# Kernel optimization log

Hardware: AMD Instinct MI355X
Metric: run time of the kernel (lower is better)

## Reference

```python
import jax, jax.numpy as jnp
import numpy as np

D_MODEL = 1024
N_HEADS = 16
HEAD_DIM = D_MODEL // N_HEADS
B, S = 2, 2048


def setup_inputs() -> dict:
    key = jax.random.key(0)
    ks = jax.random.split(key, 6)
    scale = 1.0 / np.sqrt(D_MODEL)
    inputs = jax.random.normal(ks[0], (B, S, D_MODEL), dtype=jnp.float32)
    # causal mask: 1.0 where attention is disallowed (strictly upper triangular)
    mask = jnp.triu(jnp.ones((S, S), dtype=jnp.float32), k=1)[None, None, :, :]
    mask = jnp.broadcast_to(mask, (B, 1, S, S))
    Wq = jax.random.normal(ks[1], (D_MODEL, D_MODEL), dtype=jnp.float32) * scale
    Wk = jax.random.normal(ks[2], (D_MODEL, D_MODEL), dtype=jnp.float32) * scale
    Wv = jax.random.normal(ks[3], (D_MODEL, D_MODEL), dtype=jnp.float32) * scale
    Wo = jax.random.normal(ks[4], (D_MODEL, D_MODEL), dtype=jnp.float32) * scale
    z = jnp.zeros((D_MODEL,), dtype=jnp.float32)
    return {"inputs": inputs, "mask": mask, "Wq": Wq, "bq": z, "Wk": Wk,
            "bk": z, "Wv": Wv, "bv": z, "Wo": Wo, "bo": z}


def _split_heads(x):
    b, s, _ = x.shape
    return x.reshape(b, s, N_HEADS, HEAD_DIM).transpose(0, 2, 1, 3)  # [B,H,S,Dh]


def reference(inputs, mask, Wq, bq, Wk, bk, Wv, bv, Wo, bo):
    q = _split_heads(inputs @ Wq + bq)
    k = _split_heads(inputs @ Wk + bk)
    v = _split_heads(inputs @ Wv + bv)
    # scaled dot-product attention with additive big-negative mask
    logits = jnp.einsum('bhqd,bhkd->bhqk', q, k) / jnp.sqrt(
        jnp.asarray(HEAD_DIM, dtype=q.dtype))
    logits = logits + mask * jnp.asarray(-1e9, dtype=q.dtype)
    attn_prob = jax.nn.softmax(logits, axis=-1)  # [B,H,S,S]
    ctx = jnp.einsum('bhqk,bhkd->bhqd', attn_prob, v)
    ctx = ctx.transpose(0, 2, 1, 3).reshape(inputs.shape[0], -1, D_MODEL)
    outputs = ctx @ Wo + bo
    return outputs, attn_prob
```

## Files before the change

### kernel.cpp

```cpp
#include <hip/hip_runtime.h>
#include <cstdint>

namespace {

typedef __attribute__((ext_vector_type(8))) short bf16x8;
typedef __attribute__((ext_vector_type(4))) short bf16x4;
typedef __attribute__((ext_vector_type(4))) float f32x4;

constexpr int D  = 1024;
constexpr int H  = 16;
constexpr int DH = 64;
constexpr int B  = 2;
constexpr int S  = 2048;
constexpr int M  = B * S;
constexpr float SCALE_Q = 0.125f * 1.4426950408889634f;

__device__ inline unsigned short f2bf(float f) {
    union { float f; uint32_t u; } v{f};
    return (unsigned short)((v.u + 0x7fffu + ((v.u >> 16) & 1u)) >> 16);
}

__device__ inline void gload16(const void* g, void* l) {
    __builtin_amdgcn_global_load_lds(
        (const __attribute__((address_space(1))) void*)g,
        (__attribute__((address_space(3))) void*)l, 16, 0, 0);
}

__global__ __launch_bounds__(256) void pack_x(const float* __restrict__ x,
                                              unsigned short* __restrict__ xb) {
    const int i = (blockIdx.x * 256 + threadIdx.x) * 8;
    float4 a = *reinterpret_cast<const float4*>(&x[i]);
    float4 b = *reinterpret_cast<const float4*>(&x[i + 4]);
    bf16x8 o;
    o[0] = f2bf(a.x); o[1] = f2bf(a.y); o[2] = f2bf(a.z); o[3] = f2bf(a.w);
    o[4] = f2bf(b.x); o[5] = f2bf(b.y); o[6] = f2bf(b.z); o[7] = f2bf(b.w);
    *reinterpret_cast<bf16x8*>(&xb[i]) = o;
}

__global__ __launch_bounds__(256) void transpose_w4(
    const float* __restrict__ W0, const float* __restrict__ W1,
    const float* __restrict__ W2, const float* __restrict__ W3,
    unsigned short* __restrict__ WtAll)
{
    __shared__ unsigned short T[64][72];
    const int z = blockIdx.z;
    const float* W = z == 0 ? W0 : (z == 1 ? W1 : (z == 2 ? W2 : W3));
    unsigned short* Wt = WtAll + (size_t)z * D * D;
    const int n0 = blockIdx.x * 64, k0 = blockIdx.y * 64;
    const int t = threadIdx.x;
    #pragma unroll
    for (int i = 0; i < 16; ++i) {
        int idx = i * 256 + t, r = idx >> 6, c = idx & 63;
        T[r][c] = f2bf(W[(size_t)(k0 + r) * D + n0 + c]);
    }
    __syncthreads();
    #pragma unroll
    for (int i = 0; i < 16; ++i) {
        int idx = i * 256 + t, r = idx >> 6, c = idx & 63;
        Wt[(size_t)(n0 + r) * D + k0 + c] = T[c][r];
    }
}

template <int MODE>
__global__ __launch_bounds__(256) void mfma_gemm(
    const unsigned short* __restrict__ A, const unsigned short* __restrict__ Bt,
    const float* __restrict__ b0, const float* __restrict__ b1,
    const float* __restrict__ b2,
    unsigned short* __restrict__ oQ, unsigned short* __restrict__ oK,
    unsigned short* __restrict__ oVt, float* __restrict__ oF)
{
    __shared__ __align__(16) unsigned short As[128 * 64];
    __shared__ __align__(16) unsigned short Bs[128 * 64];
    const int t = threadIdx.x;
    const int lane = t & 63, w = t >> 6;
    const int wr = w >> 1, wc = w & 1;
    const int lo = lane & 15, hi = lane >> 4;
    const int m0 = blockIdx.y * 128, n0 = blockIdx.x * 128;

    f32x4 acc[4][4] = {};

    for (int k0 = 0; k0 < D; k0 += 64) {
        #pragma unroll
        for (int i = 0; i < 4; ++i) {
            const int row = i * 32 + w * 8 + (lane >> 3);
            const int gcol = ((lane & 7) * 8) ^ ((row & 7) * 8);
            gload16(&A[(size_t)(m0 + row) * D + k0 + gcol], &As[i * 2048 + w * 512]);
            gload16(&Bt[(size_t)(n0 + row) * D + k0 + gcol], &Bs[i * 2048 + w * 512]);
        }
        __syncthreads();
        #pragma unroll
        for (int kk = 0; kk < 2; ++kk) {
            bf16x8 a[4], b[4];
            #pragma unroll
            for (int m = 0; m < 4; ++m) {
                const int row = wr * 64 + m * 16 + lo;
                a[m] = *reinterpret_cast<const bf16x8*>(
                    &As[row * 64 + ((kk * 32 + hi * 8) ^ ((row & 7) * 8))]);
            }
            #pragma unroll
            for (int n = 0; n < 4; ++n) {
                const int row = wc * 64 + n * 16 + lo;
                b[n] = *reinterpret_cast<const bf16x8*>(
                    &Bs[row * 64 + ((kk * 32 + hi * 8) ^ ((row & 7) * 8))]);
            }
            #pragma unroll
            for (int m = 0; m < 4; ++m)
                #pragma unroll
                for (int n = 0; n < 4; ++n)
                    acc[m][n] = __builtin_amdgcn_mfma_f32_16x16x32_bf16(a[m], b[n], acc[m][n], 0, 0, 0);
        }
        __syncthreads();
    }

    if (MODE == 0) {
        const int which = n0 >> 10;
        if (which == 2) {
            #pragma unroll
            for (int m = 0; m < 4; ++m) {
                const int row0 = m0 + wr * 64 + m * 16 + hi * 4;
                const int b_ = row0 >> 11, s_ = row0 & (S - 1);
                #pragma unroll
                for (int n = 0; n < 4; ++n) {
                    const int nn = (n0 + wc * 64 + n * 16 + lo) & 1023;
                    const int h_ = nn >> 6, dh = nn & 63;
                    const float bcol = b2[nn];
                    bf16x4 o;
                    #pragma unroll
                    for (int r = 0; r < 4; ++r) o[r] = (short)f2bf(acc[m][n][r] + bcol);
                    *reinterpret_cast<bf16x4*>(
                        &oVt[((size_t)(b_ * H + h_) * DH + dh) * S + s_]) = o;
                }
            }
        } else {
            const float* bs = which == 0 ? b0 : b1;
            unsigned short* op = which == 0 ? oQ : oK;
            const float scale = which == 0 ? SCALE_Q : 1.0f;
            #pragma unroll
            for (int m = 0; m < 4; ++m)
                #pragma unroll
                for (int n = 0; n < 4; ++n) {
                    const int nn = (n0 + wc * 64 + n * 16 + lo) & 1023;
                    const float bcol = bs[nn];
                    const int h_ = nn >> 6, dh = nn & 63;
                    #pragma unroll
                    for (int r = 0; r < 4; ++r) {
                        const int row = m0 + wr * 64 + m * 16 + hi * 4 + r;
                        const int b_ = row >> 11, s_ = row & (S - 1);
                        op[(((size_t)(b_ * H + h_) * S) + s_) * DH + dh] =
                            f2bf((acc[m][n][r] + bcol) * scale);
                    }
                }
        }
    } else {
        #pragma unroll
        for (int m = 0; m < 4; ++m)
            #pragma unroll
            for (int n = 0; n < 4; ++n) {
                const int col = n0 + wc * 64 + n * 16 + lo;
                const float bcol = b0[col];
                #pragma unroll
                for (int r = 0; r < 4; ++r) {
                    const int row = m0 + wr * 64 + m * 16 + hi * 4 + r;
                    oF[(size_t)row * D + col] = acc[m][n][r] + bcol;
                }
            }
    }
}

__global__ __launch_bounds__(256) void attn_fused(
    const unsigned short* __restrict__ Q, const unsigned short* __restrict__ K,
    const unsigned short* __restrict__ Vt, float* __restrict__ P,
    unsigned short* __restrict__ ctxb)
{
    __shared__ __align__(16) float Pf[2][4][16][68];
    const int bh = blockIdx.x;
    const int y = blockIdx.y;
    const int jy = y & 7, ky = y >> 3;
    const int qt = (ky == 0) ? 31 - jy : (ky == 1) ? jy : (ky == 2) ? 23 - jy : 8 + jy;
    const int t = threadIdx.x, lane = t & 63, w = t >> 6;
    const int lo = lane & 15, hi = lane >> 4;
    const int q0 = qt * 64 + w * 16;
    const unsigned short* Qb = Q + (size_t)bh * S * DH;
    const unsigned short* Kb = K + (size_t)bh * S * DH;
    const unsigned short* Vb = Vt + (size_t)bh * DH * S;
    float* Pb = P + (size_t)bh * S * S;

    bf16x8 aq[2];
    #pragma unroll
    for (int kk = 0; kk < 2; ++kk)
        aq[kk] = *reinterpret_cast<const bf16x8*>(&Qb[(size_t)(q0 + lo) * DH + kk * 32 + hi * 8]);

    float li[4];
    {
        float rsum[4] = {0.f, 0.f, 0.f, 0.f};
        for (int jt = 0; jt < qt; ++jt) {
            f32x4 acc[4] = {};
            #pragma unroll
            for (int kk = 0; kk < 2; ++kk)
                #pragma unroll
                for (int n = 0; n < 4; ++n) {
                    bf16x8 bk = *reinterpret_cast<const bf16x8*>(
                        &Kb[(size_t)(jt * 64 + n * 16 + lo) * DH + kk * 32 + hi * 8]);
                    acc[n] = __builtin_amdgcn_mfma_f32_16x16x32_bf16(aq[kk], bk, acc[n], 0, 0, 0);
                }
            #pragma unroll
            for (int n = 0; n < 4; ++n)
                #pragma unroll
                for (int r = 0; r < 4; ++r) rsum[r] += exp2f(acc[n][r]);
        }
        {
            f32x4 acc[4] = {};
            #pragma unroll
            for (int kk = 0; kk < 2; ++kk)
                #pragma unroll
                for (int n = 0; n < 4; ++n) {
                    bf16x8 bk = *reinterpret_cast<const bf16x8*>(
                        &Kb[(size_t)(qt * 64 + n * 16 + lo) * DH + kk * 32 + hi * 8]);
                    acc[n] = __builtin_amdgcn_mfma_f32_16x16x32_bf16(aq[kk], bk, acc[n], 0, 0, 0);
                }
            #pragma unroll
            for (int n = 0; n < 4; ++n) {
                const int j = qt * 64 + n * 16 + lo;
                #pragma unroll
                for (int r = 0; r < 4; ++r) {
                    const float e = exp2f(acc[n][r]);
                    rsum[r] += (j > q0 + hi * 4 + r) ? 0.f : e;
                }
            }
        }
        #pragma unroll
        for (int r = 0; r < 4; ++r) {
            #pragma unroll
            for (int off = 1; off < 16; off <<= 1) rsum[r] += __shfl_xor(rsum[r], off);
            li[r] = 1.0f / rsum[r];
        }
    }

    f32x4 actx[4] = {};

    for (int jt = 0; jt <= qt; ++jt) {
        float (*pf)[68] = Pf[jt & 1][w];
        f32x4 acc[4] = {};
        #pragma unroll
        for (int kk = 0; kk < 2; ++kk)
            #pragma unroll
            for (int n = 0; n < 4; ++n) {
                bf16x8 bk = *reinterpret_cast<const bf16x8*>(
                    &Kb[(size_t)(jt * 64 + n * 16 + lo) * DH + kk * 32 + hi * 8]);
                acc[n] = __builtin_amdgcn_mfma_f32_16x16x32_bf16(aq[kk], bk, acc[n], 0, 0, 0);
            }
        if (jt < qt) {
            #pragma unroll
            for (int n = 0; n < 4; ++n)
                #pragma unroll
                for (int r = 0; r < 4; ++r)
                    pf[hi * 4 + r][n * 16 + lo] = exp2f(acc[n][r]) * li[r];
        } else {
            #pragma unroll
            for (int n = 0; n < 4; ++n) {
                const int j = qt * 64 + n * 16 + lo;
                #pragma unroll
                for (int r = 0; r < 4; ++r) {
                    const int qrow = q0 + hi * 4 + r;
                    float p = exp2f(acc[n][r]) * li[r];
                    pf[hi * 4 + r][n * 16 + lo] = (j > qrow) ? 0.f : p;
                }
            }
        }
        #pragma unroll
        for (int i2 = 0; i2 < 4; ++i2) {
            const int row = i2 * 4 + hi;
            f32x4 v = *reinterpret_cast<const f32x4*>(&pf[row][lo * 4]);
            __builtin_nontemporal_store(
                v, reinterpret_cast<f32x4*>(&Pb[(size_t)(q0 + row) * S + jt * 64 + lo * 4]));
        }
        #pragma unroll
        for (int kk = 0; kk < 2; ++kk) {
            const float* src = &pf[lo][kk * 32 + hi * 8];
            float4 f0 = *reinterpret_cast<const float4*>(src);
            float4 f1 = *reinterpret_cast<const float4*>(src + 4);
            bf16x8 pa;
            pa[0] = f2bf(f0.x); pa[1] = f2bf(f0.y); pa[2] = f2bf(f0.z); pa[3] = f2bf(f0.w);
            pa[4] = f2bf(f1.x); pa[5] = f2bf(f1.y); pa[6] = f2bf(f1.z); pa[7] = f2bf(f1.w);
            #pragma unroll
            for (int n2 = 0; n2 < 4; ++n2) {
                bf16x8 bv = *reinterpret_cast<const bf16x8*>(
                    &Vb[(size_t)(n2 * 16 + lo) * S + jt * 64 + kk * 32 + hi * 8]);
                actx[n2] = __builtin_amdgcn_mfma_f32_16x16x32_bf16(pa, bv, actx[n2], 0, 0, 0);
            }
        }
    }

    const f32x4 z = {0.f, 0.f, 0.f, 0.f};
    for (int jt = qt + 1; jt < S / 64; ++jt)
        #pragma unroll
        for (int rr = 0; rr < 4; ++rr) {
            const int qrow = q0 + rr * 4 + hi;
            __builtin_nontemporal_store(
                z, reinterpret_cast<f32x4*>(&Pb[(size_t)qrow * S + jt * 64 + lo * 4]));
        }

    const int b_ = bh >> 4, h_ = bh & 15;
    #pragma unroll
    for (int n2 = 0; n2 < 4; ++n2)
        #pragma unroll
        for (int r = 0; r < 4; ++r) {
            const int qg = q0 + hi * 4 + r;
            ctxb[((size_t)(b_ * S + qg)) * D + h_ * 64 + n2 * 16 + lo] = f2bf(actx[n2][r]);
        }
}

}

extern "C" void kernel_launch(void* const* d_in, const int* in_sizes, int n_in,
                              void* d_out, int out_size, void* d_ws, size_t ws_size,
                              hipStream_t stream) {
    const float* x  = (const float*)d_in[0];
    const float* Wq = (const float*)d_in[2];
    const float* bq = (const float*)d_in[3];
    const float* Wk = (const float*)d_in[4];
    const float* bk = (const float*)d_in[5];
    const float* Wv = (const float*)d_in[6];
    const float* bv = (const float*)d_in[7];
    const float* Wo = (const float*)d_in[8];
    const float* bo = (const float*)d_in[9];

    float* out = (float*)d_out;
    float* P   = out + (size_t)M * D;

    char* ws = (char*)d_ws;
    const size_t MB = 1u << 20;
    unsigned short* xb    = (unsigned short*)(ws);
    unsigned short* WtAll = (unsigned short*)(ws + 8 * MB);
    unsigned short* Qb    = (unsigned short*)(ws + 16 * MB);
    unsigned short* Kb    = (unsigned short*)(ws + 24 * MB);
    unsigned short* Vtb   = (unsigned short*)(ws + 32 * MB);
    unsigned short* ctxb  = (unsigned short*)(ws + 40 * MB);

    const dim3 blk(256);

    pack_x<<<dim3(M * D / (256 * 8)), blk, 0, stream>>>(x, xb);
    transpose_w4<<<dim3(16, 16, 4), blk, 0, stream>>>(Wq, Wk, Wv, Wo, WtAll);

    mfma_gemm<0><<<dim3(24, M / 128), blk, 0, stream>>>(
        xb, WtAll, bq, bk, bv, Qb, Kb, Vtb, nullptr);

    attn_fused<<<dim3(B * H, S / 64), blk, 0, stream>>>(Qb, Kb, Vtb, P, ctxb);

    mfma_gemm<1><<<dim3(8, M / 128), blk, 0, stream>>>(
        ctxb, WtAll + (size_t)3 * D * D, bo, nullptr, nullptr,
        nullptr, nullptr, nullptr, out);
}
```

Baseline: 289.3 us.

## Give each attention wave two 16-row query groups to reuse K/V loads

Each wave now handles 32 query rows (two 16-row MFMA groups) instead of 16. Each block covers 128 query rows, so the grid drops from 32 to 16 blocks per head and the causal tile ordering changes. Every K and V fragment loaded from global memory feeds two MFMAs, halving K/V load traffic per query row. In exchange the kernel uses more registers and LDS, launches fewer blocks (512 total), and a 64-wide causal tile can now straddle a wave's rows, which may hurt occupancy and load balance on the many-CU device.

```diff
diff --git a/kernel.cpp b/kernel.cpp
--- a/kernel.cpp
+++ b/kernel.cpp
@@ -172,142 +172,171 @@
     const unsigned short* __restrict__ Vt, float* __restrict__ P,
     unsigned short* __restrict__ ctxb)
 {
-    __shared__ __align__(16) float Pf[2][4][16][68];
+    __shared__ __align__(16) float Pf[2][4][32][68];
     const int bh = blockIdx.x;
     const int y = blockIdx.y;
-    const int jy = y & 7, ky = y >> 3;
-    const int qt = (ky == 0) ? 31 - jy : (ky == 1) ? jy : (ky == 2) ? 23 - jy : 8 + jy;
+    const int Qt = (y < 8) ? 15 - y : y - 8;
     const int t = threadIdx.x, lane = t & 63, w = t >> 6;
     const int lo = lane & 15, hi = lane >> 4;
-    const int q0 = qt * 64 + w * 16;
+    const int qw = Qt * 128 + w * 32;
+    const int jt_w = (qw + 31) >> 6;
     const unsigned short* Qb = Q + (size_t)bh * S * DH;
     const unsigned short* Kb = K + (size_t)bh * S * DH;
     const unsigned short* Vb = Vt + (size_t)bh * DH * S;
     float* Pb = P + (size_t)bh * S * S;
 
-    bf16x8 aq[2];
+    bf16x8 aq[2][2];
     #pragma unroll
-    for (int kk = 0; kk < 2; ++kk)
-        aq[kk] = *reinterpret_cast<const bf16x8*>(&Qb[(size_t)(q0 + lo) * DH + kk * 32 + hi * 8]);
-
-    float li[4];
+    for (int g = 0; g < 2; ++g)
+        #pragma unroll
+        for (int kk = 0; kk < 2; ++kk)
+            aq[g][kk] = *reinterpret_cast<const bf16x8*>(
+                &Qb[(size_t)(qw + g * 16 + lo) * DH + kk * 32 + hi * 8]);
+
+    float li[2][4];
     {
-        float rsum[4] = {0.f, 0.f, 0.f, 0.f};
-        for (int jt = 0; jt < qt; ++jt) {
-            f32x4 acc[4] = {};
+        float rsum[2][4] = {};
+        for (int jt = 0; jt < jt_w; ++jt) {
+            f32x4 acc[2][4] = {};
             #pragma unroll
             for (int kk = 0; kk < 2; ++kk)
                 #pragma unroll
                 for (int n = 0; n < 4; ++n) {
                     bf16x8 bk = *reinterpret_cast<const bf16x8*>(
                         &Kb[(size_t)(jt * 64 + n * 16 + lo) * DH + kk * 32 + hi * 8]);
-                    acc[n] = __builtin_amdgcn_mfma_f32_16x16x32_bf16(aq[kk], bk, acc[n], 0, 0, 0);
-                }
-            #pragma unroll
-            for (int n = 0; n < 4; ++n)
-                #pragma unroll
-                for (int r = 0; r < 4; ++r) rsum[r] += exp2f(acc[n][r]);
+                    #pragma unroll
+                    for (int g = 0; g < 2; ++g)
+                        acc[g][n] = __builtin_amdgcn_mfma_f32_16x16x32_bf16(aq[g][kk], bk, acc[g][n], 0, 0, 0);
+                }
+            #pragma unroll
+            for (int g = 0; g < 2; ++g)
+                #pragma unroll
+                for (int n = 0; n < 4; ++n)
+                    #pragma unroll
+                    for (int r = 0; r < 4; ++r) rsum[g][r] += exp2f(acc[g][n][r]);
         }
         {
-            f32x4 acc[4] = {};
+            f32x4 acc[2][4] = {};
             #pragma unroll
             for (int kk = 0; kk < 2; ++kk)
                 #pragma unroll
                 for (int n = 0; n < 4; ++n) {
                     bf16x8 bk = *reinterpret_cast<const bf16x8*>(
-                        &Kb[(size_t)(qt * 64 + n * 16 + lo) * DH + kk * 32 + hi * 8]);
-                    acc[n] = __builtin_amdgcn_mfma_f32_16x16x32_bf16(aq[kk], bk, acc[n], 0, 0, 0);
-                }
-            #pragma unroll
-            for (int n = 0; n < 4; ++n) {
-                const int j = qt * 64 + n * 16 + lo;
-                #pragma unroll
-                for (int r = 0; r < 4; ++r) {
-                    const float e = exp2f(acc[n][r]);
-                    rsum[r] += (j > q0 + hi * 4 + r) ? 0.f : e;
-                }
-            }
-        }
-        #pragma unroll
-        for (int r = 0; r < 4; ++r) {
-            #pragma unroll
-            for (int off = 1; off < 16; off <<= 1) rsum[r] += __shfl_xor(rsum[r], off);
-            li[r] = 1.0f / rsum[r];
-        }
-    }
-
-    f32x4 actx[4] = {};
-
-    for (int jt = 0; jt <= qt; ++jt) {
+                        &Kb[(size_t)(jt_w * 64 + n * 16 + lo) * DH + kk * 32 + hi * 8]);
+                    #pragma unroll
+                    for (int g = 0; g < 2; ++g)
+                        acc[g][n] = __builtin_amdgcn_mfma_f32_16x16x32_bf16(aq[g][kk], bk, acc[g][n], 0, 0, 0);
+                }
+            #pragma unroll
+            for (int n = 0; n < 4; ++n) {
+                const int j = jt_w * 64 + n * 16 + lo;
+                #pragma unroll
+                for (int g = 0; g < 2; ++g)
+                    #pragma unroll
+                    for (int r = 0; r < 4; ++r) {
+                        const float e = exp2f(acc[g][n][r]);
+                        rsum[g][r] += (j > qw + g * 16 + hi * 4 + r) ? 0.f : e;
+                    }
+            }
+        }
+        #pragma unroll
+        for (int g = 0; g < 2; ++g)
+            #pragma unroll
+            for (int r = 0; r < 4; ++r) {
+                #pragma unroll
+                for (int off = 1; off < 16; off <<= 1)
+                    rsum[g][r] += __shfl_xor(rsum[g][r], off);
+                li[g][r] = 1.0f / rsum[g][r];
+            }
+    }
+
+    f32x4 actx[2][4] = {};
+
+    for (int jt = 0; jt <= jt_w; ++jt) {
         float (*pf)[68] = Pf[jt & 1][w];
-        f32x4 acc[4] = {};
+        f32x4 acc[2][4] = {};
         #pragma unroll
         for (int kk = 0; kk < 2; ++kk)
             #pragma unroll
             for (int n = 0; n < 4; ++n) {
                 bf16x8 bk = *reinterpret_cast<const bf16x8*>(
                     &Kb[(size_t)(jt * 64 + n * 16 + lo) * DH + kk * 32 + hi * 8]);
-                acc[n] = __builtin_amdgcn_mfma_f32_16x16x32_bf16(aq[kk], bk, acc[n], 0, 0, 0);
-            }
-        if (jt < qt) {
-            #pragma unroll
-            for (int n = 0; n < 4; ++n)
-                #pragma unroll
-                for (int r = 0; r < 4; ++r)
-                    pf[hi * 4 + r][n * 16 + lo] = exp2f(acc[n][r]) * li[r];
+                #pragma unroll
+                for (int g = 0; g < 2; ++g)
+                    acc[g][n] = __builtin_amdgcn_mfma_f32_16x16x32_bf16(aq[g][kk], bk, acc[g][n], 0, 0, 0);
+            }
+        if (jt < jt_w) {
+            #pragma unroll
+            for (int g = 0; g < 2; ++g)
+                #pragma unroll
+                for (int n = 0; n < 4; ++n)
+                    #pragma unroll
+                    for (int r = 0; r < 4; ++r)
+                        pf[g * 16 + hi * 4 + r][n * 16 + lo] = exp2f(acc[g][n][r]) * li[g][r];
         } else {
             #pragma unroll
             for (int n = 0; n < 4; ++n) {
-                const int j = qt * 64 + n * 16 + lo;
-                #pragma unroll
-                for (int r = 0; r < 4; ++r) {
-                    const int qrow = q0 + hi * 4 + r;
-                    float p = exp2f(acc[n][r]) * li[r];
-                    pf[hi * 4 + r][n * 16 + lo] = (j > qrow) ? 0.f : p;
-                }
-            }
-        }
-        #pragma unroll
-        for (int i2 = 0; i2 < 4; ++i2) {
+                const int j = jt_w * 64 + n * 16 + lo;
+                #pragma unroll
+                for (int g = 0; g < 2; ++g)
+                    #pragma unroll
+                    for (int r = 0; r < 4; ++r) {
+                        float p = exp2f(acc[g][n][r]) * li[g][r];
+                        pf[g * 16 + hi * 4 + r][n * 16 + lo] =
+                            (j > qw + g * 16 + hi * 4 + r) ? 0.f : p;
+                    }
+            }
+        }
+        #pragma unroll
+        for (int i2 = 0; i2 < 8; ++i2) {
             const int row = i2 * 4 + hi;
             f32x4 v = *reinterpret_cast<const f32x4*>(&pf[row][lo * 4]);
             __builtin_nontemporal_store(
-                v, reinterpret_cast<f32x4*>(&Pb[(size_t)(q0 + row) * S + jt * 64 + lo * 4]));
+                v, reinterpret_cast<f32x4*>(&Pb[(size_t)(qw + row) * S + jt * 64 + lo * 4]));
         }
         #pragma unroll
         for (int kk = 0; kk < 2; ++kk) {
-            const float* src = &pf[lo][kk * 32 + hi * 8];
-            float4 f0 = *reinterpret_cast<const float4*>(src);
-            float4 f1 = *reinterpret_cast<const float4*>(src + 4);
-            bf16x8 pa;
-            pa[0] = f2bf(f0.x); pa[1] = f2bf(f0.y); pa[2] = f2bf(f0.z); pa[3] = f2bf(f0.w);
-            pa[4] = f2bf(f1.x); pa[5] = f2bf(f1.y); pa[6] = f2bf(f1.z); pa[7] = f2bf(f1.w);
+            bf16x8 pa[2];
+            #pragma unroll
+            for (int g = 0; g < 2; ++g) {
+                const float* src = &pf[g * 16 + lo][kk * 32 + hi * 8];
+                float4 f0 = *reinterpret_cast<const float4*>(src);
+                float4 f1 = *reinterpret_cast<const float4*>(src + 4);
+                pa[g][0] = f2bf(f0.x); pa[g][1] = f2bf(f0.y);
+                pa[g][2] = f2bf(f0.z); pa[g][3] = f2bf(f0.w);
+                pa[g][4] = f2bf(f1.x); pa[g][5] = f2bf(f1.y);
+                pa[g][6] = f2bf(f1.z); pa[g][7] = f2bf(f1.w);
+            }
             #pragma unroll
             for (int n2 = 0; n2 < 4; ++n2) {
                 bf16x8 bv = *reinterpret_cast<const bf16x8*>(
                     &Vb[(size_t)(n2 * 16 + lo) * S + jt * 64 + kk * 32 + hi * 8]);
-                actx[n2] = __builtin_amdgcn_mfma_f32_16x16x32_bf16(pa, bv, actx[n2], 0, 0, 0);
+                #pragma unroll
+                for (int g = 0; g < 2; ++g)
+                    actx[g][n2] = __builtin_amdgcn_mfma_f32_16x16x32_bf16(pa[g], bv, actx[g][n2], 0, 0, 0);
             }
         }
     }
 
     const f32x4 z = {0.f, 0.f, 0.f, 0.f};
-    for (int jt = qt + 1; jt < S / 64; ++jt)
-        #pragma unroll
-        for (int rr = 0; rr < 4; ++rr) {
-            const int qrow = q0 + rr * 4 + hi;
+    for (int jt = jt_w + 1; jt < S / 64; ++jt)
+        #pragma unroll
+        for (int rr = 0; rr < 8; ++rr) {
+            const int qrow = qw + rr * 4 + hi;
             __builtin_nontemporal_store(
                 z, reinterpret_cast<f32x4*>(&Pb[(size_t)qrow * S + jt * 64 + lo * 4]));
         }
 
     const int b_ = bh >> 4, h_ = bh & 15;
     #pragma unroll
-    for (int n2 = 0; n2 < 4; ++n2)
-        #pragma unroll
-        for (int r = 0; r < 4; ++r) {
-            const int qg = q0 + hi * 4 + r;
-            ctxb[((size_t)(b_ * S + qg)) * D + h_ * 64 + n2 * 16 + lo] = f2bf(actx[n2][r]);
-        }
+    for (int g = 0; g < 2; ++g)
+        #pragma unroll
+        for (int n2 = 0; n2 < 4; ++n2)
+            #pragma unroll
+            for (int r = 0; r < 4; ++r) {
+                const int qg = qw + g * 16 + hi * 4 + r;
+                ctxb[((size_t)(b_ * S + qg)) * D + h_ * 64 + n2 * 16 + lo] = f2bf(actx[g][n2][r]);
+            }
 }
 
 }
@@ -345,7 +374,7 @@
     mfma_gemm<0><<<dim3(24, M / 128), blk, 0, stream>>>(
         xb, WtAll, bq, bk, bv, Qb, Kb, Vtb, nullptr);
 
-    attn_fused<<<dim3(B * H, S / 64), blk, 0, stream>>>(Qb, Kb, Vtb, P, ctxb);
+    attn_fused<<<dim3(B * H, 16), blk, 0, stream>>>(Qb, Kb, Vtb, P, ctxb);
 
     mfma_gemm<1><<<dim3(8, M / 128), blk, 0, stream>>>(
         ctxb, WtAll + (size_t)3 * D * D, bo, nullptr, nullptr,
```

New measurement: 243.1 us (median of 2 runs). 16.0% less time.
